# Optimization experiments

Hardware: AMD Instinct MI355X
Metric: run time of the kernel (lower is better)

## Reference

```python
import jax, jax.numpy as jnp
import numpy as np

N_NODES = 20000
N_EDGES = 320000
IN_DIM = 128
HID = 256
HEADS = 8
DH = HID // HEADS  # 32
LAYERS = 3
NUM_GRAPHS = 64
OUT_DIM = 10
SLOPE = 0.2  # DGL GATv2Conv default negative_slope


def setup_inputs() -> dict:
    key = jax.random.key(0)
    ks = jax.random.split(key, 20)
    s_in = 1.0 / np.sqrt(IN_DIM)
    s_h = 1.0 / np.sqrt(HID)
    s_h2 = 1.0 / np.sqrt(HID // 2)
    return {
        "feature": jax.random.normal(ks[0], (N_NODES, IN_DIM), jnp.float32),
        "W_in": jax.random.normal(ks[1], (IN_DIM, HID), jnp.float32) * s_in,
        "b_in": jax.random.normal(ks[2], (HID,), jnp.float32) * 0.01,
        "W_src": jax.random.normal(ks[3], (LAYERS, HID, HID), jnp.float32) * s_h,
        "b_src": jax.random.normal(ks[4], (LAYERS, HID), jnp.float32) * 0.01,
        "W_dst": jax.random.normal(ks[5], (LAYERS, HID, HID), jnp.float32) * s_h,
        "b_dst": jax.random.normal(ks[6], (LAYERS, HID), jnp.float32) * 0.01,
        "attn": jax.random.normal(ks[7], (LAYERS, HEADS, DH), jnp.float32) * (1.0 / np.sqrt(DH)),
        "Wc1": jax.random.normal(ks[8], (HID, HID), jnp.float32) * s_h,
        "bc1": jax.random.normal(ks[9], (HID,), jnp.float32) * 0.01,
        "Wc2": jax.random.normal(ks[10], (HID, HID // 2), jnp.float32) * s_h,
        "bc2": jax.random.normal(ks[11], (HID // 2,), jnp.float32) * 0.01,
        "Wc3": jax.random.normal(ks[12], (HID // 2, OUT_DIM), jnp.float32) * s_h2,
        "bc3": jax.random.normal(ks[13], (OUT_DIM,), jnp.float32) * 0.01,
        "src": jax.random.randint(ks[14], (N_EDGES,), 0, N_NODES, jnp.int32),
        "dst": jax.random.randint(ks[15], (N_EDGES,), 0, N_NODES, jnp.int32),
        "graph_ids": jnp.sort(jax.random.randint(ks[16], (N_NODES,), 0, NUM_GRAPHS, jnp.int32)),
    }


def _gatv2_layer(h, Ws, bs, Wd, bd, a, src, dst):
    # DGL GATv2Conv: e_ij = a^T LeakyReLU(W_src h_j + W_dst h_i), edge softmax over
    # incoming edges of dst, scatter-sum of alpha * W_src h_src; residual = Identity
    # (in_feats == heads*out_feats); activation relu.
    n = h.shape[0]
    fs = (h @ Ws + bs).reshape(n, HEADS, DH)  # [N,H,D]
    fd = (h @ Wd + bd).reshape(n, HEADS, DH)
    e = jax.nn.leaky_relu(fs[src] + fd[dst], SLOPE)          # [E,H,D]
    score = jnp.einsum("ehd,hd->eh", e, a)                   # [E,H]
    m = jax.ops.segment_max(score, dst, num_segments=n)       # stable softmax max
    ex = jnp.exp(score - m[dst])
    denom = jax.ops.segment_sum(ex, dst, num_segments=n)
    alpha = ex / denom[dst]                                    # [E,H]
    rst = jax.ops.segment_sum(alpha[:, :, None] * fs[src], dst, num_segments=n)
    out = jax.nn.relu(rst + h.reshape(n, HEADS, DH))          # residual + activation
    return out.reshape(n, HID)


def reference(feature, W_in, b_in, W_src, b_src, W_dst, b_dst, attn,
              Wc1, bc1, Wc2, bc2, Wc3, bc3, src, dst, graph_ids):
    h = feature @ W_in + b_in
    for l in range(LAYERS):
        h = _gatv2_layer(h, W_src[l], b_src[l], W_dst[l], b_dst[l], attn[l], src, dst)
    # dgl.sum_nodes over batched graph -> per-graph segment sum
    hg = jax.ops.segment_sum(h, graph_ids, num_segments=NUM_GRAPHS)  # [G,HID]
    # classifier (dropout is identity in eval mode)
    x = jax.nn.relu(hg @ Wc1 + bc1)
    x = jax.nn.relu(x @ Wc2 + bc2)
    return x @ Wc3 + bc3  # [G,OUT_DIM]
```

## Files before the change

### kernel.cpp

```cpp
#include <hip/hip_runtime.h>
#include <hip/hip_bf16.h>
#include <math.h>

#define N_NODES 20000
#define N_EDGES 320000
#define IN_DIM 128
#define HID 256
#define HEADS 8
#define DH 32
#define LAYERS 3
#define NUM_GRAPHS 64
#define OUT_DIM 10
#define SLOPE 0.2f

#define NBKT 5
#define N_BINS (N_NODES * NBKT)
#define N_BINS4 (N_BINS / 4)

#define CHUNK_I4 255
#define N_CHUNKS 99

#define GEMM_TILES 626
#define COUNT_BLOCKS 1250

typedef __bf16 bf16x8 __attribute__((ext_vector_type(8)));
typedef float f32x4 __attribute__((ext_vector_type(4)));

static __device__ __forceinline__ unsigned short f2bfbits(float v) {
    __bf16 b = (__bf16)v;
    return __builtin_bit_cast(unsigned short, b);
}
static __device__ __forceinline__ void unpack8(uint4 u, float* f) {
    unsigned p0 = u.x, p1 = u.y, p2 = u.z, p3 = u.w;
    f[0] = __builtin_bit_cast(float, p0 << 16);
    f[1] = __builtin_bit_cast(float, p0 & 0xffff0000u);
    f[2] = __builtin_bit_cast(float, p1 << 16);
    f[3] = __builtin_bit_cast(float, p1 & 0xffff0000u);
    f[4] = __builtin_bit_cast(float, p2 << 16);
    f[5] = __builtin_bit_cast(float, p2 & 0xffff0000u);
    f[6] = __builtin_bit_cast(float, p3 << 16);
    f[7] = __builtin_bit_cast(float, p3 & 0xffff0000u);
}

typedef const __attribute__((address_space(1))) unsigned int* as1_u32p;
typedef __attribute__((address_space(3))) unsigned int* as3_u32p;
static __device__ __forceinline__ void async_cp16(const unsigned short* g, unsigned short* l) {
    __builtin_amdgcn_global_load_lds((as1_u32p)g, (as3_u32p)l, 16, 0, 0);
}

#define CAST_N4 (N_NODES * IN_DIM / 4)
#define WTRANS_TOTAL (IN_DIM * HID + 6 * HID * HID)
#define PREP_TOTAL (CAST_N4 + WTRANS_TOTAL)
#define PREP_BLOCKS (PREP_TOTAL / 256)

static __device__ void prep_item(int idx,
                                 const float* __restrict__ feat,
                                 const float* __restrict__ Win,
                                 const float* __restrict__ Wsrc,
                                 const float* __restrict__ Wdst,
                                 unsigned short* __restrict__ featH,
                                 unsigned short* __restrict__ WinT,
                                 unsigned short* __restrict__ WT) {
    if (idx < CAST_N4) {
        float4 v = ((const float4*)feat)[idx];
        ushort4 o;
        o.x = f2bfbits(v.x); o.y = f2bfbits(v.y);
        o.z = f2bfbits(v.z); o.w = f2bfbits(v.w);
        ((ushort4*)featH)[idx] = o;
    } else {
        int j = idx - CAST_N4;
        if (j < IN_DIM * HID) {
            int n = j / IN_DIM, k = j % IN_DIM;
            WinT[j] = f2bfbits(Win[k * HID + n]);
        } else {
            int r6 = j - IN_DIM * HID;
            int mat = r6 >> 16;
            int r = r6 & 65535;
            int n = r >> 8, k = r & 255;
            const float* base = (mat < 3) ? (Wsrc + (size_t)mat * 65536)
                                          : (Wdst + (size_t)(mat - 3) * 65536);
            WT[r6] = f2bfbits(base[k * 256 + n]);
        }
    }
}

static __device__ void scans_unit(int u, int t, const int* __restrict__ cnt,
                                  int* __restrict__ cglob, int* __restrict__ offs,
                                  int* __restrict__ cursor, int* si) {
    int idx4 = u * CHUNK_I4 + t;
    bool act = (t < CHUNK_I4) && (idx4 < N_BINS4);
    int4 x = make_int4(0, 0, 0, 0);
    if (act) x = ((const int4*)cnt)[idx4];
    int tsum = x.x + x.y + x.z + x.w;
    int v = tsum;
#pragma unroll
    for (int d = 1; d < 64; d <<= 1) {
        int w = __shfl_up(v, d, 64);
        if ((t & 63) >= d) v += w;
    }
    if ((t & 63) == 63) si[4 + (t >> 6)] = v;
    __syncthreads();
    if (t == 0) {
        int S = si[4] + si[5] + si[6] + si[7];
        si[0] = atomicAdd(cglob, S);
    }
    __syncthreads();
    int base = si[0];
    int wid = t >> 6;
    int waveoff = 0;
    if (wid > 0) waveoff += si[4];
    if (wid > 1) waveoff += si[5];
    if (wid > 2) waveoff += si[6];
    int ex = base + waveoff + (v - tsum);
    if (act) {
        int4 o;
        o.x = ex; o.y = ex + x.x; o.z = o.y + x.y; o.w = o.z + x.z;
        ((int4*)offs)[idx4] = o;
        ((int4*)cursor)[idx4] = o;
    }
}

template <int DUAL>
static __device__ void gemm_tile(int mt, int nt, int t,
                                 const unsigned short* __restrict__ Ah,
                                 const unsigned short* __restrict__ BT1,
                                 const float* __restrict__ bias1,
                                 unsigned short* __restrict__ O1,
                                 const unsigned short* __restrict__ BT2,
                                 const float* __restrict__ bias2,
                                 unsigned short* __restrict__ O2,
                                 int M, int K, int N,
                                 unsigned short* Bs1P, unsigned short* Bs2P) {
    const int wv = t >> 6, lane = t & 63, quad = lane >> 4, l15 = lane & 15;
    const int m0 = mt * 64, n0 = nt * 128;

    const int sB0 = wv * 64 + lane, sB1v = sB0 + 256;
    const int rB0 = sB0 >> 2, cB0 = (sB0 & 3) ^ ((rB0 >> 1) & 3);
    const int rB1 = sB1v >> 2, cB1 = (sB1v & 3) ^ ((rB1 >> 1) & 3);
    const size_t offB0 = (size_t)(n0 + rB0) * K + cB0 * 8;
    const size_t offB1 = (size_t)(n0 + rB1) * K + cB1 * 8;

    auto issueB = [&](int buf, int k0) {
        async_cp16(BT1 + offB0 + k0, Bs1P + buf * 4096 + wv * 512);
        async_cp16(BT1 + offB1 + k0, Bs1P + buf * 4096 + 2048 + wv * 512);
        if (DUAL) {
            async_cp16(BT2 + offB0 + k0, Bs2P + buf * 4096 + wv * 512);
            async_cp16(BT2 + offB1 + k0, Bs2P + buf * 4096 + 2048 + wv * 512);
        }
    };

    const int mrow0 = (wv >> 1) * 32;
    const int ncb = (wv & 1) * 64;

    int r0 = m0 + mrow0 + l15;      if (r0 >= M) r0 = M - 1;
    int r1 = m0 + mrow0 + 16 + l15; if (r1 >= M) r1 = M - 1;
    const unsigned short* Ap0 = Ah + (size_t)r0 * K + quad * 8;
    const unsigned short* Ap1 = Ah + (size_t)r1 * K + quad * 8;

    f32x4 zero = {0.f, 0.f, 0.f, 0.f};
    f32x4 acc1[2][4], acc2[2][4];
#pragma unroll
    for (int mi = 0; mi < 2; ++mi)
#pragma unroll
        for (int t4 = 0; t4 < 4; ++t4) { acc1[mi][t4] = zero; acc2[mi][t4] = zero; }

    issueB(0, 0);
    bf16x8 aC0 = __builtin_bit_cast(bf16x8, *(const uint4*)(Ap0));
    bf16x8 aC1 = __builtin_bit_cast(bf16x8, *(const uint4*)(Ap1));

    int buf = 0;
    for (int k0 = 0; k0 < K; k0 += 32, buf ^= 1) {
        __syncthreads();
        bf16x8 aN0 = aC0, aN1 = aC1;
        if (k0 + 32 < K) {
            issueB(buf ^ 1, k0 + 32);
            aN0 = __builtin_bit_cast(bf16x8, *(const uint4*)(Ap0 + k0 + 32));
            aN1 = __builtin_bit_cast(bf16x8, *(const uint4*)(Ap1 + k0 + 32));
        }
#pragma unroll
        for (int t4 = 0; t4 < 4; ++t4) {
            int brow = ncb + t4 * 16 + l15;
            int boff = brow * 32 + ((quad ^ ((brow >> 1) & 3)) << 3);
            bf16x8 b1 = __builtin_bit_cast(bf16x8, *(const uint4*)(Bs1P + buf * 4096 + boff));
            acc1[0][t4] = __builtin_amdgcn_mfma_f32_16x16x32_bf16(aC0, b1, acc1[0][t4], 0, 0, 0);
            acc1[1][t4] = __builtin_amdgcn_mfma_f32_16x16x32_bf16(aC1, b1, acc1[1][t4], 0, 0, 0);
            if (DUAL) {
                bf16x8 b2 = __builtin_bit_cast(bf16x8, *(const uint4*)(Bs2P + buf * 4096 + boff));
                acc2[0][t4] = __builtin_amdgcn_mfma_f32_16x16x32_bf16(aC0, b2, acc2[0][t4], 0, 0, 0);
                acc2[1][t4] = __builtin_amdgcn_mfma_f32_16x16x32_bf16(aC1, b2, acc2[1][t4], 0, 0, 0);
            }
        }
        aC0 = aN0; aC1 = aN1;
    }

    float bia1[4], bia2[4];
#pragma unroll
    for (int t4 = 0; t4 < 4; ++t4) {
        bia1[t4] = bias1[n0 + ncb + t4 * 16 + l15];
        bia2[t4] = DUAL ? bias2[n0 + ncb + t4 * 16 + l15] : 0.f;
    }
#pragma unroll
    for (int mi = 0; mi < 2; ++mi) {
#pragma unroll
        for (int t4 = 0; t4 < 4; ++t4) {
            int gn = n0 + ncb + t4 * 16 + l15;
#pragma unroll
            for (int r = 0; r < 4; ++r) {
                int gm = m0 + mrow0 + mi * 16 + quad * 4 + r;
                if (gm < M) {
                    float v = acc1[mi][t4][r] + bia1[t4];
                    O1[(size_t)gm * N + gn] = f2bfbits(v);
                    if (DUAL) {
                        float v2 = acc2[mi][t4][r] + bia2[t4];
                        O2[(size_t)gm * N + gn] = f2bfbits(v2);
                    }
                }
            }
        }
    }
}

static __device__ void agg_unit(int u, int t,
                                const unsigned short* __restrict__ fsb,
                                const unsigned short* __restrict__ fdb,
                                unsigned short* __restrict__ hb,
                                const int* __restrict__ offs,
                                const int* __restrict__ cnt,
                                const int* __restrict__ csr_src,
                                const float* __restrict__ attn_l) {
    int node = u * 8 + (t >> 5);
    if (node >= N_NODES) return;
    int l32 = t & 31;
    int dbase = l32 * 8;
    int abase = (l32 >> 2) * DH + (l32 & 3) * 8;

    float a[8];
#pragma unroll
    for (int j = 0; j < 8; ++j) a[j] = attn_l[abase + j];

    float fdv[8];
    unpack8(*(const uint4*)(fdb + (size_t)node * HID + dbase), fdv);

    float ssum0 = 0.f, ssum1 = 0.f;
    float acc0[8], acc1[8];
#pragma unroll
    for (int j = 0; j < 8; ++j) { acc0[j] = 0.f; acc1[j] = 0.f; }

    auto procE = [&](uint4 uu, float* acc, float& ssum) {
        float fsv[8];
        unpack8(uu, fsv);
        float p = 0.f;
#pragma unroll
        for (int j = 0; j < 8; ++j) {
            float e = fsv[j] + fdv[j];
            e = fmaxf(e, SLOPE * e);
            p += e * a[j];
        }
        p += __shfl_xor(p, 1, 64);
        p += __shfl_xor(p, 2, 64);
        float w = __expf(p);
        ssum += w;
#pragma unroll
        for (int j = 0; j < 8; ++j) acc[j] += w * fsv[j];
    };

    const unsigned short* fsl = fsb + dbase;
    int b0 = node * NBKT;
    int beg = offs[b0];
    int end = offs[b0 + NBKT - 1] + cnt[b0 + NBKT - 1];
    int nfull = (end - beg) >> 2;
    const int limit = beg + nfull * 4;

    uint4 cu0, cu1, cu2, cu3;
    int ci0, ci1, ci2, ci3;
    int base = beg + 8;
    bool have = (nfull >= 1);
    bool haveN = (nfull >= 2);
    if (have) {
        int s0 = csr_src[beg], s1 = csr_src[beg + 1];
        int s2 = csr_src[beg + 2], s3 = csr_src[beg + 3];
        if (haveN) {
            ci0 = csr_src[beg + 4]; ci1 = csr_src[beg + 5];
            ci2 = csr_src[beg + 6]; ci3 = csr_src[beg + 7];
        }
        cu0 = *(const uint4*)(fsl + (size_t)s0 * HID);
        cu1 = *(const uint4*)(fsl + (size_t)s1 * HID);
        cu2 = *(const uint4*)(fsl + (size_t)s2 * HID);
        cu3 = *(const uint4*)(fsl + (size_t)s3 * HID);
    }
    while (have) {
        uint4 nu0, nu1, nu2, nu3;
        int ni0, ni1, ni2, ni3;
        if (haveN) {
            nu0 = *(const uint4*)(fsl + (size_t)ci0 * HID);
            nu1 = *(const uint4*)(fsl + (size_t)ci1 * HID);
            nu2 = *(const uint4*)(fsl + (size_t)ci2 * HID);
            nu3 = *(const uint4*)(fsl + (size_t)ci3 * HID);
        }
        bool haveNN = (base + 4 <= limit);
        if (haveNN) {
            ni0 = csr_src[base]; ni1 = csr_src[base + 1];
            ni2 = csr_src[base + 2]; ni3 = csr_src[base + 3];
        }
        base += 4;
        procE(cu0, acc0, ssum0);
        procE(cu1, acc1, ssum1);
        procE(cu2, acc0, ssum0);
        procE(cu3, acc1, ssum1);
        if (haveN) { cu0 = nu0; cu1 = nu1; cu2 = nu2; cu3 = nu3; }
        if (haveNN) { ci0 = ni0; ci1 = ni1; ci2 = ni2; ci3 = ni3; }
        have = haveN; haveN = haveNN;
    }
    for (int idx = limit; idx < end; ++idx) {
        int sv = csr_src[idx];
        procE(*(const uint4*)(fsl + (size_t)sv * HID), acc0, ssum0);
    }

    float ssum = ssum0 + ssum1;
    float acc[8];
#pragma unroll
    for (int j = 0; j < 8; ++j) acc[j] = acc0[j] + acc1[j];

    float inv = ssum > 0.f ? 1.f / ssum : 0.f;
    float hv[8];
    unpack8(*(const uint4*)(hb + (size_t)node * HID + dbase), hv);
    unsigned short ob[8];
#pragma unroll
    for (int j = 0; j < 8; ++j) {
        float o = fmaxf(acc[j] * inv + hv[j], 0.f);
        ob[j] = f2bfbits(o);
    }
    *(uint4*)(hb + (size_t)node * HID + dbase) = *(uint4*)ob;
}

__global__ void prep_count_kernel(const float* __restrict__ feat,
                                  const float* __restrict__ Win,
                                  const float* __restrict__ Wsrc,
                                  const float* __restrict__ Wdst,
                                  unsigned short* __restrict__ featH,
                                  unsigned short* __restrict__ WinT,
                                  unsigned short* __restrict__ WT,
                                  const int* __restrict__ src,
                                  const int* __restrict__ dst,
                                  int* __restrict__ cnt) {
    int bid = blockIdx.x;
    if (bid < PREP_BLOCKS) {
        prep_item(bid * 256 + threadIdx.x, feat, Win, Wsrc, Wdst, featH, WinT, WT);
    } else {
        int e = (bid - PREP_BLOCKS) * 256 + threadIdx.x;
        if (e < N_EDGES) atomicAdd(&cnt[dst[e] * NBKT + (src[e] >> 12)], 1);
    }
}

__global__ __launch_bounds__(256, 4) void gemm0_scan_kernel(
    const unsigned short* __restrict__ featH, const unsigned short* __restrict__ WinT,
    const float* __restrict__ b_in, unsigned short* __restrict__ hb,
    const int* __restrict__ cnt, int* __restrict__ cglob,
    int* __restrict__ offs, int* __restrict__ cursor) {
    __shared__ __align__(16) unsigned short smem[8192];
    int bid = blockIdx.x;
    if (bid < GEMM_TILES) {
        gemm_tile<0>(bid >> 1, bid & 1, threadIdx.x, featH, WinT, b_in, hb,
                     (const unsigned short*)nullptr, (const float*)nullptr,
                     (unsigned short*)nullptr, N_NODES, IN_DIM, HID,
                     smem, smem);
    } else {
        scans_unit(bid - GEMM_TILES, threadIdx.x, cnt, cglob, offs, cursor,
                   (int*)(void*)smem);
    }
}

__global__ __launch_bounds__(256, 4) void gemm1_fill_kernel(
    const unsigned short* __restrict__ hb,
    const unsigned short* __restrict__ WTs, const float* __restrict__ bs,
    unsigned short* __restrict__ fsb,
    const unsigned short* __restrict__ WTd, const float* __restrict__ bd,
    unsigned short* __restrict__ fdb,
    const int* __restrict__ src, const int* __restrict__ dst,
    int* __restrict__ cursor, int* __restrict__ csr_src) {
    __shared__ __align__(16) unsigned short smem[16384];
    int bid = blockIdx.x;
    if (bid < GEMM_TILES) {
        gemm_tile<1>(bid >> 1, bid & 1, threadIdx.x, hb, WTs, bs, fsb, WTd, bd, fdb,
                     N_NODES, HID, HID, smem, smem + 8192);
    } else {
        int e = (bid - GEMM_TILES) * 256 + threadIdx.x;
        if (e < N_EDGES) {
            int sv = src[e];
            int p = atomicAdd(&cursor[dst[e] * NBKT + (sv >> 12)], 1);
            csr_src[p] = sv;
        }
    }
}

__global__ __launch_bounds__(256, 4) void gemm_kernel(
    const unsigned short* __restrict__ Ah,
    const unsigned short* __restrict__ BT1, const float* __restrict__ bias1,
    unsigned short* __restrict__ O1,
    const unsigned short* __restrict__ BT2, const float* __restrict__ bias2,
    unsigned short* __restrict__ O2) {
    __shared__ __align__(16) unsigned short smem[16384];
    gemm_tile<1>(blockIdx.x, blockIdx.y, threadIdx.x, Ah, BT1, bias1, O1,
                 BT2, bias2, O2, N_NODES, HID, HID, smem, smem + 8192);
}

__global__ __launch_bounds__(256) void agg_kernel(const unsigned short* __restrict__ fsb,
                                                  const unsigned short* __restrict__ fdb,
                                                  unsigned short* __restrict__ hb,
                                                  const int* __restrict__ offs,
                                                  const int* __restrict__ cnt,
                                                  const int* __restrict__ csr_src,
                                                  const float* __restrict__ attn_l) {
    int nwg = gridDim.x;
    int q = nwg >> 3, r = nwg & 7;
    int xcd = blockIdx.x & 7, idx = blockIdx.x >> 3;
    int u = (xcd < r) ? xcd * (q + 1) + idx
                      : r * (q + 1) + (xcd - r) * q + idx;
    agg_unit(u, threadIdx.x, fsb, fdb, hb, offs, cnt, csr_src, attn_l);
}

__global__ __launch_bounds__(256) void poolcls_kernel(
    const unsigned short* __restrict__ hb, const int* __restrict__ gid,
    const float* __restrict__ Wc1, const float* __restrict__ bc1,
    const float* __restrict__ Wc2, const float* __restrict__ bc2,
    const float* __restrict__ Wc3, const float* __restrict__ bc3,
    float* __restrict__ out) {
    __shared__ float part[8 * HID];
    __shared__ float xin[HID];
    __shared__ float x1[HID];
    __shared__ float x2[HID / 2];
    int g = blockIdx.x, t = threadIdx.x;

    int lo = 0, hi = N_NODES;
    while (lo < hi) { int mid = (lo + hi) >> 1; if (gid[mid] < g) lo = mid + 1; else hi = mid; }
    int s0 = lo;
    hi = N_NODES;
    while (lo < hi) { int mid = (lo + hi) >> 1; if (gid[mid] < g + 1) lo = mid + 1; else hi = mid; }
    int e0 = lo;

    int r = t >> 5;
    int fb = (t & 31) * 8;
    float a0[8], a1[8];
#pragma unroll
    for (int j = 0; j < 8; ++j) { a0[j] = 0.f; a1[j] = 0.f; }
    int n = s0 + r;
    for (; n + 8 < e0; n += 16) {
        uint4 u0 = *(const uint4*)(hb + (size_t)n * HID + fb);
        uint4 u1 = *(const uint4*)(hb + (size_t)(n + 8) * HID + fb);
        float f0[8], f1[8];
        unpack8(u0, f0); unpack8(u1, f1);
#pragma unroll
        for (int j = 0; j < 8; ++j) { a0[j] += f0[j]; a1[j] += f1[j]; }
    }
    if (n < e0) {
        uint4 u0 = *(const uint4*)(hb + (size_t)n * HID + fb);
        float f0[8];
        unpack8(u0, f0);
#pragma unroll
        for (int j = 0; j < 8; ++j) a0[j] += f0[j];
    }
#pragma unroll
    for (int j = 0; j < 8; ++j) part[r * HID + fb + j] = a0[j] + a1[j];
    __syncthreads();
    {
        float s = 0.f;
#pragma unroll
        for (int r2 = 0; r2 < 8; ++r2) s += part[r2 * HID + t];
        xin[t] = s;
    }
    __syncthreads();

    {
        float acc = bc1[t];
        for (int k = 0; k < HID; ++k) acc += xin[k] * Wc1[k * HID + t];
        x1[t] = fmaxf(acc, 0.f);
    }
    __syncthreads();
    if (t < HID / 2) {
        float acc = bc2[t];
        for (int k = 0; k < HID; ++k) acc += x1[k] * Wc2[k * (HID / 2) + t];
        x2[t] = fmaxf(acc, 0.f);
    }
    __syncthreads();
    if (t < OUT_DIM) {
        float acc = bc3[t];
        for (int k = 0; k < HID / 2; ++k) acc += x2[k] * Wc3[k * OUT_DIM + t];
        out[g * OUT_DIM + t] = acc;
    }
}

extern "C" void kernel_launch(void* const* d_in, const int* in_sizes, int n_in,
                              void* d_out, int out_size, void* d_ws, size_t ws_size,
                              hipStream_t stream) {
    const float* feature = (const float*)d_in[0];
    const float* W_in   = (const float*)d_in[1];
    const float* b_in   = (const float*)d_in[2];
    const float* W_src  = (const float*)d_in[3];
    const float* b_src  = (const float*)d_in[4];
    const float* W_dst  = (const float*)d_in[5];
    const float* b_dst  = (const float*)d_in[6];
    const float* attn   = (const float*)d_in[7];
    const float* Wc1    = (const float*)d_in[8];
    const float* bc1    = (const float*)d_in[9];
    const float* Wc2    = (const float*)d_in[10];
    const float* bc2    = (const float*)d_in[11];
    const float* Wc3    = (const float*)d_in[12];
    const float* bc3    = (const float*)d_in[13];
    const int* src     = (const int*)d_in[14];
    const int* dst     = (const int*)d_in[15];
    const int* gid     = (const int*)d_in[16];
    float* out = (float*)d_out;

    char* w = (char*)d_ws;
    auto alloc = [&](size_t bytes) -> void* {
        void* p = (void*)w;
        w += (bytes + 255) & ~(size_t)255;
        return p;
    };
    unsigned short* hb  = (unsigned short*)alloc((size_t)N_NODES * HID * 2);
    unsigned short* fsb = (unsigned short*)alloc((size_t)N_NODES * HID * 2);
    unsigned short* fdb = (unsigned short*)alloc((size_t)N_NODES * HID * 2);
    int* cnt     = (int*)alloc((size_t)N_BINS * 4);
    int* cglob   = (int*)alloc(4);
    int* offs    = (int*)alloc((size_t)(N_BINS + 4) * 4);
    int* cursor  = (int*)alloc((size_t)N_BINS * 4);
    int* csr_src = (int*)alloc((size_t)N_EDGES * 4);
    unsigned short* WinT = (unsigned short*)alloc((size_t)IN_DIM * HID * 2);
    unsigned short* WT   = (unsigned short*)alloc((size_t)6 * HID * HID * 2);
    unsigned short* featH = (unsigned short*)alloc((size_t)N_NODES * IN_DIM * 2);
    (void)alloc(4096);

    size_t zlen = (size_t)((char*)offs - (char*)cnt);
    hipMemsetAsync(cnt, 0, zlen, stream);

    hipLaunchKernelGGL(prep_count_kernel, dim3(PREP_BLOCKS + COUNT_BLOCKS), dim3(256), 0, stream,
                       feature, W_in, W_src, W_dst, featH, WinT, WT, src, dst, cnt);

    hipLaunchKernelGGL(gemm0_scan_kernel, dim3(GEMM_TILES + N_CHUNKS), dim3(256), 0, stream,
                       featH, WinT, b_in, hb, cnt, cglob, offs, cursor);

    hipLaunchKernelGGL(gemm1_fill_kernel, dim3(GEMM_TILES + COUNT_BLOCKS), dim3(256), 0, stream,
                       hb, WT, b_src, fsb, WT + 3 * 65536, b_dst, fdb,
                       src, dst, cursor, csr_src);

    for (int l = 0; l < LAYERS; ++l) {
        hipLaunchKernelGGL(agg_kernel, dim3(N_NODES / 8), dim3(256), 0, stream,
                           fsb, fdb, hb, offs, cnt, csr_src, attn + (size_t)l * HEADS * DH);
        if (l + 1 < LAYERS) {
            hipLaunchKernelGGL(gemm_kernel, dim3(313, 2), dim3(256), 0, stream,
                               hb, WT + (size_t)(l + 1) * 65536, b_src + (size_t)(l + 1) * HID, fsb,
                               WT + (size_t)(4 + l) * 65536, b_dst + (size_t)(l + 1) * HID, fdb);
        }
    }

    hipLaunchKernelGGL(poolcls_kernel, dim3(NUM_GRAPHS), dim3(256), 0, stream,
                       hb, gid, Wc1, bc1, Wc2, bc2, Wc3, bc3, out);
}
```

Measured before the change: 314.6 us.

## Load GEMM B fragments directly from global into registers, dropping LDS staging

The GEMM tile no longer stages the transposed weight tiles through double-buffered LDS via async global-to-LDS copies. Each wave now loads its own B fragments straight from global memory into registers, prefetching the next k-step, and the per-iteration __syncthreads goes away. Launch bounds drop from 4 to 2 blocks per CU to make room for the extra fragment registers. The cost is that B data shared by the waves of a block is fetched redundantly from global/L2 rather than once into LDS, and occupancy may fall.

```diff
diff --git a/kernel.cpp b/kernel.cpp
--- a/kernel.cpp
+++ b/kernel.cpp
@@ -42,10 +42,8 @@
     f[7] = __builtin_bit_cast(float, p3 & 0xffff0000u);
 }
 
-typedef const __attribute__((address_space(1))) unsigned int* as1_u32p;
-typedef __attribute__((address_space(3))) unsigned int* as3_u32p;
-static __device__ __forceinline__ void async_cp16(const unsigned short* g, unsigned short* l) {
-    __builtin_amdgcn_global_load_lds((as1_u32p)g, (as3_u32p)l, 16, 0, 0);
+static __device__ __forceinline__ bf16x8 ldfrag(const unsigned short* p) {
+    return __builtin_bit_cast(bf16x8, *(const uint4*)p);
 }
 
 #define CAST_N4 (N_NODES * IN_DIM / 4)
@@ -129,26 +127,9 @@
                                  const unsigned short* __restrict__ BT2,
                                  const float* __restrict__ bias2,
                                  unsigned short* __restrict__ O2,
-                                 int M, int K, int N,
-                                 unsigned short* Bs1P, unsigned short* Bs2P) {
+                                 int M, int K, int N) {
     const int wv = t >> 6, lane = t & 63, quad = lane >> 4, l15 = lane & 15;
     const int m0 = mt * 64, n0 = nt * 128;
-
-    const int sB0 = wv * 64 + lane, sB1v = sB0 + 256;
-    const int rB0 = sB0 >> 2, cB0 = (sB0 & 3) ^ ((rB0 >> 1) & 3);
-    const int rB1 = sB1v >> 2, cB1 = (sB1v & 3) ^ ((rB1 >> 1) & 3);
-    const size_t offB0 = (size_t)(n0 + rB0) * K + cB0 * 8;
-    const size_t offB1 = (size_t)(n0 + rB1) * K + cB1 * 8;
-
-    auto issueB = [&](int buf, int k0) {
-        async_cp16(BT1 + offB0 + k0, Bs1P + buf * 4096 + wv * 512);
-        async_cp16(BT1 + offB1 + k0, Bs1P + buf * 4096 + 2048 + wv * 512);
-        if (DUAL) {
-            async_cp16(BT2 + offB0 + k0, Bs2P + buf * 4096 + wv * 512);
-            async_cp16(BT2 + offB1 + k0, Bs2P + buf * 4096 + 2048 + wv * 512);
-        }
-    };
-
     const int mrow0 = (wv >> 1) * 32;
     const int ncb = (wv & 1) * 64;
 
@@ -157,6 +138,15 @@
     const unsigned short* Ap0 = Ah + (size_t)r0 * K + quad * 8;
     const unsigned short* Ap1 = Ah + (size_t)r1 * K + quad * 8;
 
+    const unsigned short* B1p[4];
+    const unsigned short* B2p[4];
+#pragma unroll
+    for (int t4 = 0; t4 < 4; ++t4) {
+        int brow = n0 + ncb + t4 * 16 + l15;
+        B1p[t4] = BT1 + (size_t)brow * K + quad * 8;
+        if (DUAL) B2p[t4] = BT2 + (size_t)brow * K + quad * 8;
+    }
+
     f32x4 zero = {0.f, 0.f, 0.f, 0.f};
     f32x4 acc1[2][4], acc2[2][4];
 #pragma unroll
@@ -164,33 +154,43 @@
 #pragma unroll
         for (int t4 = 0; t4 < 4; ++t4) { acc1[mi][t4] = zero; acc2[mi][t4] = zero; }
 
-    issueB(0, 0);
-    bf16x8 aC0 = __builtin_bit_cast(bf16x8, *(const uint4*)(Ap0));
-    bf16x8 aC1 = __builtin_bit_cast(bf16x8, *(const uint4*)(Ap1));
-
-    int buf = 0;
-    for (int k0 = 0; k0 < K; k0 += 32, buf ^= 1) {
-        __syncthreads();
-        bf16x8 aN0 = aC0, aN1 = aC1;
-        if (k0 + 32 < K) {
-            issueB(buf ^ 1, k0 + 32);
-            aN0 = __builtin_bit_cast(bf16x8, *(const uint4*)(Ap0 + k0 + 32));
-            aN1 = __builtin_bit_cast(bf16x8, *(const uint4*)(Ap1 + k0 + 32));
+    bf16x8 aC0 = ldfrag(Ap0), aC1 = ldfrag(Ap1);
+    bf16x8 bC1[4], bC2[4];
+#pragma unroll
+    for (int t4 = 0; t4 < 4; ++t4) {
+        bC1[t4] = ldfrag(B1p[t4]);
+        if (DUAL) bC2[t4] = ldfrag(B2p[t4]);
+    }
+
+    for (int k0 = 0; k0 < K; k0 += 32) {
+        bf16x8 aN0, aN1, bN1[4], bN2[4];
+        bool more = (k0 + 32 < K);
+        if (more) {
+            aN0 = ldfrag(Ap0 + k0 + 32);
+            aN1 = ldfrag(Ap1 + k0 + 32);
+#pragma unroll
+            for (int t4 = 0; t4 < 4; ++t4) {
+                bN1[t4] = ldfrag(B1p[t4] + k0 + 32);
+                if (DUAL) bN2[t4] = ldfrag(B2p[t4] + k0 + 32);
+            }
         }
 #pragma unroll
         for (int t4 = 0; t4 < 4; ++t4) {
-            int brow = ncb + t4 * 16 + l15;
-            int boff = brow * 32 + ((quad ^ ((brow >> 1) & 3)) << 3);
-            bf16x8 b1 = __builtin_bit_cast(bf16x8, *(const uint4*)(Bs1P + buf * 4096 + boff));
-            acc1[0][t4] = __builtin_amdgcn_mfma_f32_16x16x32_bf16(aC0, b1, acc1[0][t4], 0, 0, 0);
-            acc1[1][t4] = __builtin_amdgcn_mfma_f32_16x16x32_bf16(aC1, b1, acc1[1][t4], 0, 0, 0);
+            acc1[0][t4] = __builtin_amdgcn_mfma_f32_16x16x32_bf16(aC0, bC1[t4], acc1[0][t4], 0, 0, 0);
+            acc1[1][t4] = __builtin_amdgcn_mfma_f32_16x16x32_bf16(aC1, bC1[t4], acc1[1][t4], 0, 0, 0);
             if (DUAL) {
-                bf16x8 b2 = __builtin_bit_cast(bf16x8, *(const uint4*)(Bs2P + buf * 4096 + boff));
-                acc2[0][t4] = __builtin_amdgcn_mfma_f32_16x16x32_bf16(aC0, b2, acc2[0][t4], 0, 0, 0);
-                acc2[1][t4] = __builtin_amdgcn_mfma_f32_16x16x32_bf16(aC1, b2, acc2[1][t4], 0, 0, 0);
+                acc2[0][t4] = __builtin_amdgcn_mfma_f32_16x16x32_bf16(aC0, bC2[t4], acc2[0][t4], 0, 0, 0);
+                acc2[1][t4] = __builtin_amdgcn_mfma_f32_16x16x32_bf16(aC1, bC2[t4], acc2[1][t4], 0, 0, 0);
             }
         }
-        aC0 = aN0; aC1 = aN1;
+        if (more) {
+            aC0 = aN0; aC1 = aN1;
+#pragma unroll
+            for (int t4 = 0; t4 < 4; ++t4) {
+                bC1[t4] = bN1[t4];
+                if (DUAL) bC2[t4] = bN2[t4];
+            }
+        }
     }
 
     float bia1[4], bia2[4];
@@ -352,25 +352,23 @@
     }
 }
 
-__global__ __launch_bounds__(256, 4) void gemm0_scan_kernel(
+__global__ __launch_bounds__(256, 2) void gemm0_scan_kernel(
     const unsigned short* __restrict__ featH, const unsigned short* __restrict__ WinT,
     const float* __restrict__ b_in, unsigned short* __restrict__ hb,
     const int* __restrict__ cnt, int* __restrict__ cglob,
     int* __restrict__ offs, int* __restrict__ cursor) {
-    __shared__ __align__(16) unsigned short smem[8192];
+    __shared__ int si[8];
     int bid = blockIdx.x;
     if (bid < GEMM_TILES) {
         gemm_tile<0>(bid >> 1, bid & 1, threadIdx.x, featH, WinT, b_in, hb,
                      (const unsigned short*)nullptr, (const float*)nullptr,
-                     (unsigned short*)nullptr, N_NODES, IN_DIM, HID,
-                     smem, smem);
+                     (unsigned short*)nullptr, N_NODES, IN_DIM, HID);
     } else {
-        scans_unit(bid - GEMM_TILES, threadIdx.x, cnt, cglob, offs, cursor,
-                   (int*)(void*)smem);
-    }
-}
-
-__global__ __launch_bounds__(256, 4) void gemm1_fill_kernel(
+        scans_unit(bid - GEMM_TILES, threadIdx.x, cnt, cglob, offs, cursor, si);
+    }
+}
+
+__global__ __launch_bounds__(256, 2) void gemm1_fill_kernel(
     const unsigned short* __restrict__ hb,
     const unsigned short* __restrict__ WTs, const float* __restrict__ bs,
     unsigned short* __restrict__ fsb,
@@ -378,11 +376,10 @@
     unsigned short* __restrict__ fdb,
     const int* __restrict__ src, const int* __restrict__ dst,
     int* __restrict__ cursor, int* __restrict__ csr_src) {
-    __shared__ __align__(16) unsigned short smem[16384];
     int bid = blockIdx.x;
     if (bid < GEMM_TILES) {
         gemm_tile<1>(bid >> 1, bid & 1, threadIdx.x, hb, WTs, bs, fsb, WTd, bd, fdb,
-                     N_NODES, HID, HID, smem, smem + 8192);
+                     N_NODES, HID, HID);
     } else {
         int e = (bid - GEMM_TILES) * 256 + threadIdx.x;
         if (e < N_EDGES) {
@@ -393,15 +390,14 @@
     }
 }
 
-__global__ __launch_bounds__(256, 4) void gemm_kernel(
+__global__ __launch_bounds__(256, 2) void gemm_kernel(
     const unsigned short* __restrict__ Ah,
     const unsigned short* __restrict__ BT1, const float* __restrict__ bias1,
     unsigned short* __restrict__ O1,
     const unsigned short* __restrict__ BT2, const float* __restrict__ bias2,
     unsigned short* __restrict__ O2) {
-    __shared__ __align__(16) unsigned short smem[16384];
     gemm_tile<1>(blockIdx.x, blockIdx.y, threadIdx.x, Ah, BT1, bias1, O1,
-                 BT2, bias2, O2, N_NODES, HID, HID, smem, smem + 8192);
+                 BT2, bias2, O2, N_NODES, HID, HID);
 }
 
 __global__ __launch_bounds__(256) void agg_kernel(const unsigned short* __restrict__ fsb,
```

Result: slower. 365.4 us (+16.1%).
